# Kernel tuning notes

Hardware: AMD Instinct MI355X
Metric: run time of the kernel (lower is better)

## Reference

```python
import jax, jax.numpy as jnp
import numpy as np


def gcn_conv(x, src, dst, W, b, n_nodes):
    """PyG-style GCNConv: add self-loops, symmetric deg^-1/2 normalization,
    linear transform, scatter-add aggregation to dst, then bias."""
    loop = jnp.arange(n_nodes, dtype=src.dtype)
    s = jnp.concatenate([src, loop])
    d = jnp.concatenate([dst, loop])
    deg = jax.ops.segment_sum(jnp.ones_like(d, x.dtype), d, num_segments=n_nodes)
    dinv = jax.lax.rsqrt(deg)  # deg >= 1 due to self-loops
    norm = dinv[s] * dinv[d]  # [E+N]
    h = x @ W.T  # [N, out]
    msg = h[s] * norm[:, None]  # [E+N, out]
    return jax.ops.segment_sum(msg, d, num_segments=n_nodes) + b


def setup_inputs() -> dict:
    key = jax.random.key(0)
    k = jax.random.split(key, 6)
    N, E, IN, HID, OUT = 100000, 1600000, 128, 128, 64
    x = jax.random.normal(k[0], (N, IN), dtype=jnp.float32)
    edge_index = jax.random.randint(k[1], (2, E), 0, N, dtype=jnp.int64)
    W1 = jax.random.normal(k[2], (HID, IN), dtype=jnp.float32) * 0.05
    b1 = jnp.zeros((HID,), dtype=jnp.float32)
    W2 = jax.random.normal(k[3], (OUT, HID), dtype=jnp.float32) * 0.05
    b2 = jnp.zeros((OUT,), dtype=jnp.float32)
    return {"x": x, "W1": W1, "b1": b1, "W2": W2, "b2": b2, "edge_index": edge_index}


def reference(x, W1, b1, W2, b2, edge_index):
    n_nodes = x.shape[0]
    src, dst = edge_index[0], edge_index[1]
    h = jax.nn.relu(gcn_conv(x, src, dst, W1, b1, n_nodes))
    return gcn_conv(h, src, dst, W2, b2, n_nodes)
```

## Files before the change

### kernel.cpp

```cpp
#include <hip/hip_runtime.h>
#include <hip/hip_bf16.h>


#define IN_F  128
#define HID_F 128
#define OUT_F 64

#define NPB     512
#define MAXBKT  256
#define CHUNK   4096
#define SLAB    12288
#define CAP     12288

typedef __bf16 bf16_t;
typedef __bf16 bf16x4 __attribute__((ext_vector_type(4)));
typedef __bf16 bf16x8 __attribute__((ext_vector_type(8)));
typedef float  f32x2  __attribute__((ext_vector_type(2)));
typedef float  f32x4  __attribute__((ext_vector_type(4)));
typedef unsigned u32x2 __attribute__((ext_vector_type(2)));
typedef unsigned u32x4 __attribute__((ext_vector_type(4)));

__global__ __launch_bounds__(256) void k_hist(const int* __restrict__ dst, int E,
                                              int* __restrict__ chunkhist, int NBKT,
                                              int pchunks,
                                              const float* __restrict__ W1s,
                                              const float* __restrict__ W2s,
                                              bf16_t* __restrict__ Wdst,
                                              int n1, int n2,
                                              int* __restrict__ bcur) {
    if ((int)blockIdx.x >= pchunks) {
        int i = (blockIdx.x - pchunks) * 256 + threadIdx.x;
        if (i < n1) Wdst[i] = (bf16_t)W1s[i];
        else if (i < n1 + n2) Wdst[i] = (bf16_t)W2s[i - n1];
        else if (i < n1 + n2 + NBKT) bcur[(i - n1 - n2) * 16] = (i - n1 - n2) * SLAB;
        return;
    }
    __shared__ int cnt[MAXBKT];
    for (int i = threadIdx.x; i < NBKT; i += 256) cnt[i] = 0;
    __syncthreads();
    int base = blockIdx.x * CHUNK;
    for (int i = threadIdx.x; i < CHUNK; i += 256) {
        int e = base + i;
        if (e < E) atomicAdd(&cnt[dst[e] >> 9], 1);
    }
    __syncthreads();
    int* ch = chunkhist + (size_t)blockIdx.x * MAXBKT;
    for (int i = threadIdx.x; i < NBKT; i += 256) ch[i] = cnt[i];
}

__global__ __launch_bounds__(256) void k_part(const int* __restrict__ src,
                                              const int* __restrict__ dst, int E,
                                              int* __restrict__ bcur,
                                              const int* __restrict__ chunkhist,
                                              unsigned* __restrict__ part, int NBKT) {
    __shared__ int cnt[MAXBKT];
    __shared__ int base[MAXBKT];
    const int* ch = chunkhist + (size_t)blockIdx.x * MAXBKT;
    int off = (int)((blockIdx.x * 73u) % (unsigned)NBKT);
    for (int j = threadIdx.x; j < NBKT; j += 256) {
        int i = j + off; if (i >= NBKT) i -= NBKT;
        int c = ch[i];
        base[i] = c ? atomicAdd(&bcur[i * 16], c) : 0;
        cnt[i] = 0;
    }
    __syncthreads();
    int cbase = blockIdx.x * CHUNK;
    for (int i = threadIdx.x; i < CHUNK; i += 256) {
        int e = cbase + i;
        if (e < E) {
            int d = dst[e];
            int b = d >> 9;
            int lp = atomicAdd(&cnt[b], 1);
            part[base[b] + lp] = (unsigned)src[e] | ((unsigned)(d & 511) << 17);
        }
    }
}

__global__ __launch_bounds__(256) void k_bucket(const unsigned* __restrict__ part,
                                                const int* __restrict__ bcur,
                                                int2* __restrict__ off2,
                                                int* __restrict__ col,
                                                float* __restrict__ dinv, int N) {
    __shared__ int lcnt[NPB];
    __shared__ int lexc[NPB];
    __shared__ int lcur[NPB];
    __shared__ int psum[256];
    __shared__ int stage[CAP];
    int b = blockIdx.x;
    int t = threadIdx.x;
    int node0 = b * NPB;
    int e0s = b * SLAB;
    int cnt = bcur[b * 16] - e0s;
    for (int i = t; i < NPB; i += 256) lcnt[i] = 0;
    __syncthreads();
    for (int i = t; i < cnt; i += 256)
        atomicAdd(&lcnt[part[e0s + i] >> 17], 1);
    __syncthreads();
    int n2b = t * 2;
    int pc0 = (lcnt[n2b] + 7) & ~7;
    int pc1 = (lcnt[n2b + 1] + 7) & ~7;
    psum[t] = pc0 + pc1;
    __syncthreads();
    for (int ofs = 1; ofs < 256; ofs <<= 1) {
        int add = (t >= ofs) ? psum[t - ofs] : 0;
        __syncthreads();
        psum[t] += add;
        __syncthreads();
    }
    int run = (t > 0) ? psum[t - 1] : 0;
    {
        lexc[n2b] = run; lcur[n2b] = run;
        int node = node0 + n2b;
        if (node < N) {
            off2[node] = make_int2(e0s + run, e0s + run + pc0);
            dinv[node] = rsqrtf((float)lcnt[n2b] + 1.0f);
        }
        run += pc0;
        lexc[n2b + 1] = run; lcur[n2b + 1] = run;
        node = node0 + n2b + 1;
        if (node < N) {
            off2[node] = make_int2(e0s + run, e0s + run + pc1);
            dinv[node] = rsqrtf((float)lcnt[n2b + 1] + 1.0f);
        }
    }
    __syncthreads();
    for (int i = t; i < cnt; i += 256) {
        unsigned p = part[e0s + i];
        int dl = p >> 17;
        int sv = (int)(p & 0x1FFFF);
        int lp = atomicAdd(&lcur[dl], 1);
        if (lp < CAP) stage[lp] = sv;
        else col[e0s + lp] = sv;
    }
    __syncthreads();
#pragma unroll
    for (int j = 0; j < 2; j++) {
        int idx = n2b + j;
        int en = lexc[idx] + ((lcnt[idx] + 7) & ~7);
        for (int i = lcur[idx]; i < en; i++) {
            if (i < CAP) stage[i] = N; else col[e0s + i] = N;
        }
    }
    __syncthreads();
    int tot = psum[255];
    for (int i = t; i < tot && i < CAP; i += 256) col[e0s + i] = stage[i];
}

template <int NCOL, typename TIN>
__global__ __launch_bounds__(256) void k_gemm_mfma(const TIN* __restrict__ X,
                                                   const bf16_t* __restrict__ W,
                                                   const float* __restrict__ scale,
                                                   bf16_t* __restrict__ H, int N) {
    constexpr int CT = NCOL / 16;
    int wv = threadIdx.x >> 6, lane = threadIdx.x & 63;
    int quad = lane >> 4, l16 = lane & 15;
    int row0 = blockIdx.x * 128 + wv * 32;
    f32x4 acc[2][CT] = {};
#pragma unroll
    for (int ks = 0; ks < 4; ks++) {
        int k0 = ks * 32 + quad * 8;
        bf16x8 a[2];
#pragma unroll
        for (int rt = 0; rt < 2; rt++) {
            int r = row0 + rt * 16 + l16;
            if (r >= N) r = N - 1;
            const TIN* p = X + (size_t)r * 128 + k0;
            if constexpr (sizeof(TIN) == 4) {
                f32x4 x0 = *(const f32x4*)p;
                f32x4 x1 = *(const f32x4*)(p + 4);
                bf16x8 tt;
                tt[0] = (bf16_t)x0[0]; tt[1] = (bf16_t)x0[1];
                tt[2] = (bf16_t)x0[2]; tt[3] = (bf16_t)x0[3];
                tt[4] = (bf16_t)x1[0]; tt[5] = (bf16_t)x1[1];
                tt[6] = (bf16_t)x1[2]; tt[7] = (bf16_t)x1[3];
                a[rt] = tt;
            } else {
                a[rt] = *(const bf16x8*)p;
            }
        }
#pragma unroll
        for (int ct = 0; ct < CT; ct++) {
            bf16x8 bfrag = *(const bf16x8*)(W + (size_t)(ct * 16 + l16) * 128 + k0);
#pragma unroll
            for (int rt = 0; rt < 2; rt++)
                acc[rt][ct] = __builtin_amdgcn_mfma_f32_16x16x32_bf16(a[rt], bfrag, acc[rt][ct], 0, 0, 0);
        }
    }
#pragma unroll
    for (int rt = 0; rt < 2; rt++)
#pragma unroll
        for (int r4 = 0; r4 < 4; r4++) {
            int r = row0 + rt * 16 + quad * 4 + r4;
            if (r < N) {
                float sc = scale[r];
#pragma unroll
                for (int ct = 0; ct < CT; ct++)
                    H[(size_t)r * NCOL + ct * 16 + l16] = (bf16_t)(sc * acc[rt][ct][r4]);
            } else if (r == N) {
#pragma unroll
                for (int ct = 0; ct < CT; ct++)
                    H[(size_t)N * NCOL + ct * 16 + l16] = (bf16_t)0.f;
            }
        }
}

template <int ROWE>
__device__ __forceinline__ void gather8(const bf16_t* __restrict__ hp,
                                        const int* __restrict__ col, int e,
                                        u32x4* w) {
    int4 c0 = *(const int4*)(col + e);
    int4 c1 = *(const int4*)(col + e + 4);
    w[0] = *(const u32x4*)(hp + (unsigned)c0.x * (unsigned)ROWE);
    w[1] = *(const u32x4*)(hp + (unsigned)c0.y * (unsigned)ROWE);
    w[2] = *(const u32x4*)(hp + (unsigned)c0.z * (unsigned)ROWE);
    w[3] = *(const u32x4*)(hp + (unsigned)c0.w * (unsigned)ROWE);
    w[4] = *(const u32x4*)(hp + (unsigned)c1.x * (unsigned)ROWE);
    w[5] = *(const u32x4*)(hp + (unsigned)c1.y * (unsigned)ROWE);
    w[6] = *(const u32x4*)(hp + (unsigned)c1.z * (unsigned)ROWE);
    w[7] = *(const u32x4*)(hp + (unsigned)c1.w * (unsigned)ROWE);
}

__device__ __forceinline__ void accum8(const u32x4* w, f32x2* a2) {
#pragma unroll
    for (int u = 0; u < 8; u++)
#pragma unroll
        for (int k = 0; k < 4; k++) {
            f32x2 v;
            v.x = __uint_as_float(w[u][k] << 16);
            v.y = __uint_as_float(w[u][k] & 0xffff0000u);
            a2[k] += v;
        }
}

__global__ __launch_bounds__(256) void k_agg_gemm(const bf16_t* __restrict__ h,
                                                  const int2* __restrict__ off2,
                                                  const int* __restrict__ col,
                                                  const float* __restrict__ dinv,
                                                  const float* __restrict__ bias,
                                                  const bf16_t* __restrict__ W2,
                                                  bf16_t* __restrict__ h2, int N) {
    __shared__ float hl[16][132];
    __shared__ float dl[16];
    int lane = threadIdx.x & 63;
    int wv = threadIdx.x >> 6;
    int g = lane >> 4, fl = lane & 15;
    int node0 = blockIdx.x * 16;
    int node = node0 + wv * 4 + g;
    bool alive = node < N;
    int f = fl * 8;
    const bf16_t* hp = h + f;
    f32x2 a2[4] = {};
    float di = 0.f;
    if (alive) {
        u32x4 ws = *(const u32x4*)(hp + (unsigned)node * 128u);
        int2 oe = off2[node];
        di = dinv[node];
#pragma unroll
        for (int k = 0; k < 4; k++) {
            f32x2 v;
            v.x = __uint_as_float(ws[k] << 16);
            v.y = __uint_as_float(ws[k] & 0xffff0000u);
            a2[k] = v;
        }
        u32x4 w[8];
        for (int e = oe.x; e < oe.y; e += 8) {
            gather8<128>(hp, col, e, w);
            accum8(w, a2);
        }
    }
    f32x4 b0 = *(const f32x4*)(bias + f);
    f32x4 b1 = *(const f32x4*)(bias + f + 4);
    int lr = wv * 4 + g;
#pragma unroll
    for (int j = 0; j < 8; j++) {
        float bv = (j < 4) ? b0[j] : b1[j - 4];
        float val = a2[j >> 1][j & 1] * di + bv;
        hl[lr][f + j] = fmaxf(val, 0.f);
    }
    if (fl == 0) dl[lr] = di;
    __syncthreads();

    int quad = lane >> 4, l16 = lane & 15;
    f32x4 c4 = {0.f, 0.f, 0.f, 0.f};
#pragma unroll
    for (int ks = 0; ks < 4; ks++) {
        int k0 = ks * 32 + quad * 8;
        bf16x8 afr;
#pragma unroll
        for (int j = 0; j < 8; j++) afr[j] = (bf16_t)hl[l16][k0 + j];
        bf16x8 bfr = *(const bf16x8*)(W2 + (size_t)(wv * 16 + l16) * 128 + k0);
        c4 = __builtin_amdgcn_mfma_f32_16x16x32_bf16(afr, bfr, c4, 0, 0, 0);
    }
#pragma unroll
    for (int r4 = 0; r4 < 4; r4++) {
        int rr = quad * 4 + r4;
        int gn = node0 + rr;
        if (gn < N)
            h2[(size_t)gn * 64 + wv * 16 + l16] = (bf16_t)(dl[rr] * c4[r4]);
    }
    if (blockIdx.x == 0 && threadIdx.x < 32)
        ((unsigned*)h2)[(size_t)N * 32 + threadIdx.x] = 0u;
}

template <int ROWE, int LPN, bool RELU, typename TOUT>
__global__ __launch_bounds__(256) void k_agg(const bf16_t* __restrict__ h,
                                             const int2* __restrict__ off2,
                                             const int* __restrict__ col,
                                             const float* __restrict__ dinv,
                                             const float* __restrict__ bias,
                                             TOUT* __restrict__ out, int N) {
    constexpr int NPW = 64 / LPN;
    int lane = threadIdx.x & 63;
    int wv = threadIdx.x >> 6;
    int g = lane / LPN, fl = lane % LPN;
    int node = blockIdx.x * (4 * NPW) + wv * NPW + g;
    if (node >= N) return;
    int f = fl * 8;
    const bf16_t* hp = h + f;
    u32x4 ws = *(const u32x4*)(hp + (unsigned)node * (unsigned)ROWE);
    int2 oe = off2[node];
    float di = dinv[node];
    f32x2 a2[4];
#pragma unroll
    for (int k = 0; k < 4; k++) {
        f32x2 v;
        v.x = __uint_as_float(ws[k] << 16);
        v.y = __uint_as_float(ws[k] & 0xffff0000u);
        a2[k] = v;
    }
    u32x4 w[8];
    for (int e = oe.x; e < oe.y; e += 8) {
        gather8<ROWE>(hp, col, e, w);
        accum8(w, a2);
    }
    f32x4 b0 = *(const f32x4*)(bias + f);
    f32x4 b1 = *(const f32x4*)(bias + f + 4);
    float r[8];
#pragma unroll
    for (int j = 0; j < 8; j++) {
        float bv = (j < 4) ? b0[j] : b1[j - 4];
        float val = a2[j >> 1][j & 1] * di + bv;
        if (RELU) val = fmaxf(val, 0.f);
        r[j] = val;
    }
    if constexpr (sizeof(TOUT) == 2) {
        bf16x8 v;
#pragma unroll
        for (int j = 0; j < 8; j++) v[j] = (bf16_t)r[j];
        *(bf16x8*)((bf16_t*)out + (size_t)node * ROWE + f) = v;
    } else {
        f32x4 v0 = {r[0], r[1], r[2], r[3]};
        f32x4 v1 = {r[4], r[5], r[6], r[7]};
        *(f32x4*)((float*)out + (size_t)node * ROWE + f) = v0;
        *(f32x4*)((float*)out + (size_t)node * ROWE + f + 4) = v1;
    }
}

extern "C" void kernel_launch(void* const* d_in, const int* in_sizes, int n_in,
                              void* d_out, int out_size, void* d_ws, size_t ws_size,
                              hipStream_t stream) {
    const float* x  = (const float*)d_in[0];
    const float* W1 = (const float*)d_in[1];
    const float* b1 = (const float*)d_in[2];
    const float* W2 = (const float*)d_in[3];
    const float* b2 = (const float*)d_in[4];
    const int*   ei = (const int*)d_in[5];

    int N = in_sizes[0] / IN_F;
    int E = in_sizes[5] / 2;
    const int* src = ei;
    const int* dst = ei + E;
    int NBKT = (N + NPB - 1) / NPB;
    int pchunks = (E + CHUNK - 1) / CHUNK;

    size_t woff = 0;
    auto alloc = [&](size_t bytes) {
        void* p = (char*)d_ws + woff;
        woff += (bytes + 255) & ~(size_t)255;
        return p;
    };
    int*      bcur  = (int*)alloc((size_t)NBKT * 16 * 4);
    int*      chist = (int*)alloc((size_t)pchunks * MAXBKT * 4);
    unsigned* part  = (unsigned*)alloc((size_t)NBKT * SLAB * 4);
    int*      col   = (int*)alloc((size_t)NBKT * SLAB * 4);
    int2*     off2  = (int2*)alloc((size_t)N * 8);
    float*    dinv  = (float*)alloc((size_t)N * 4);
    bf16_t*   Wb    = (bf16_t*)alloc((size_t)(HID_F * IN_F + OUT_F * HID_F) * 2);
    bf16_t*   W1b   = Wb;
    bf16_t*   W2b   = Wb + HID_F * IN_F;
    bf16_t*   h1    = (bf16_t*)alloc((size_t)(N + 1) * HID_F * 2);
    bf16_t*   h2b   = (bf16_t*)alloc((size_t)(N + 1) * OUT_F * 2);
    float*    outp  = (float*)d_out;

    int n1 = HID_F * IN_F, n2 = OUT_F * HID_F;
    int tailblocks = (n1 + n2 + NBKT + 255) / 256;
    k_hist<<<pchunks + tailblocks, 256, 0, stream>>>(dst, E, chist, NBKT, pchunks,
                                                     W1, W2, Wb, n1, n2, bcur);
    k_part<<<pchunks, 256, 0, stream>>>(src, dst, E, bcur, chist, part, NBKT);
    k_bucket<<<NBKT, 256, 0, stream>>>(part, bcur, off2, col, dinv, N);

    int gemm_blocks = (N + 127) / 128;

    k_gemm_mfma<HID_F, float><<<gemm_blocks, 256, 0, stream>>>(x, W1b, dinv, h1, N);
    k_agg_gemm<<<(N + 15) / 16, 256, 0, stream>>>(h1, off2, col, dinv, b1, W2b, h2b, N);
    k_agg<OUT_F, 8, false, float><<<(N + 31) / 32, 256, 0, stream>>>(h2b, off2, col, dinv, b2, outp, N);
}
```

Measured before the change: 266.2 us.

## Fuse histogram into partition kernel, drop weight pre-cast, widen bucket blocks

Removes the separate histogram kernel by recomputing per-chunk bucket counts inside k_part before reserving slab space with atomics, and replaces the bcur init with a memset. Weights are now read as fp32 and converted to bf16 inside the GEMM kernels instead of in a pre-pass. k_bucket uses 512 threads so each thread owns one node. This saves a launch and the chunk-histogram traffic, at the cost of reading dst twice in k_part and extra conversion work and fp32 weight loads in the GEMMs.

Result: slower. 271.6 us (+2.1%).

```diff
diff --git a/kernel.cpp b/kernel.cpp
--- a/kernel.cpp
+++ b/kernel.cpp
@@ -20,63 +20,36 @@
 typedef unsigned u32x2 __attribute__((ext_vector_type(2)));
 typedef unsigned u32x4 __attribute__((ext_vector_type(4)));
 
-__global__ __launch_bounds__(256) void k_hist(const int* __restrict__ dst, int E,
-                                              int* __restrict__ chunkhist, int NBKT,
-                                              int pchunks,
-                                              const float* __restrict__ W1s,
-                                              const float* __restrict__ W2s,
-                                              bf16_t* __restrict__ Wdst,
-                                              int n1, int n2,
-                                              int* __restrict__ bcur) {
-    if ((int)blockIdx.x >= pchunks) {
-        int i = (blockIdx.x - pchunks) * 256 + threadIdx.x;
-        if (i < n1) Wdst[i] = (bf16_t)W1s[i];
-        else if (i < n1 + n2) Wdst[i] = (bf16_t)W2s[i - n1];
-        else if (i < n1 + n2 + NBKT) bcur[(i - n1 - n2) * 16] = (i - n1 - n2) * SLAB;
-        return;
-    }
-    __shared__ int cnt[MAXBKT];
-    for (int i = threadIdx.x; i < NBKT; i += 256) cnt[i] = 0;
-    __syncthreads();
-    int base = blockIdx.x * CHUNK;
-    for (int i = threadIdx.x; i < CHUNK; i += 256) {
-        int e = base + i;
-        if (e < E) atomicAdd(&cnt[dst[e] >> 9], 1);
-    }
-    __syncthreads();
-    int* ch = chunkhist + (size_t)blockIdx.x * MAXBKT;
-    for (int i = threadIdx.x; i < NBKT; i += 256) ch[i] = cnt[i];
-}
-
 __global__ __launch_bounds__(256) void k_part(const int* __restrict__ src,
                                               const int* __restrict__ dst, int E,
                                               int* __restrict__ bcur,
-                                              const int* __restrict__ chunkhist,
                                               unsigned* __restrict__ part, int NBKT) {
     __shared__ int cnt[MAXBKT];
     __shared__ int base[MAXBKT];
-    const int* ch = chunkhist + (size_t)blockIdx.x * MAXBKT;
+    for (int i = threadIdx.x; i < NBKT; i += 256) cnt[i] = 0;
+    __syncthreads();
+    int cbase = blockIdx.x * CHUNK;
+    int cend = min(cbase + CHUNK, E);
+    for (int e = cbase + (int)threadIdx.x; e < cend; e += 256)
+        atomicAdd(&cnt[dst[e] >> 9], 1);
+    __syncthreads();
     int off = (int)((blockIdx.x * 73u) % (unsigned)NBKT);
     for (int j = threadIdx.x; j < NBKT; j += 256) {
         int i = j + off; if (i >= NBKT) i -= NBKT;
-        int c = ch[i];
-        base[i] = c ? atomicAdd(&bcur[i * 16], c) : 0;
+        int c = cnt[i];
+        base[i] = c ? (i * SLAB + atomicAdd(&bcur[i * 16], c)) : 0;
         cnt[i] = 0;
     }
     __syncthreads();
-    int cbase = blockIdx.x * CHUNK;
-    for (int i = threadIdx.x; i < CHUNK; i += 256) {
-        int e = cbase + i;
-        if (e < E) {
-            int d = dst[e];
-            int b = d >> 9;
-            int lp = atomicAdd(&cnt[b], 1);
-            part[base[b] + lp] = (unsigned)src[e] | ((unsigned)(d & 511) << 17);
-        }
-    }
-}
-
-__global__ __launch_bounds__(256) void k_bucket(const unsigned* __restrict__ part,
+    for (int e = cbase + (int)threadIdx.x; e < cend; e += 256) {
+        int d = dst[e];
+        int b = d >> 9;
+        int lp = atomicAdd(&cnt[b], 1);
+        part[base[b] + lp] = (unsigned)src[e] | ((unsigned)(d & 511) << 17);
+    }
+}
+
+__global__ __launch_bounds__(512) void k_bucket(const unsigned* __restrict__ part,
                                                 const int* __restrict__ bcur,
                                                 int2* __restrict__ off2,
                                                 int* __restrict__ col,
@@ -84,47 +57,37 @@
     __shared__ int lcnt[NPB];
     __shared__ int lexc[NPB];
     __shared__ int lcur[NPB];
-    __shared__ int psum[256];
+    __shared__ int psum[NPB];
     __shared__ int stage[CAP];
     int b = blockIdx.x;
     int t = threadIdx.x;
     int node0 = b * NPB;
     int e0s = b * SLAB;
-    int cnt = bcur[b * 16] - e0s;
-    for (int i = t; i < NPB; i += 256) lcnt[i] = 0;
-    __syncthreads();
-    for (int i = t; i < cnt; i += 256)
+    int cnt = bcur[b * 16];
+    lcnt[t] = 0;
+    __syncthreads();
+    for (int i = t; i < cnt; i += 512)
         atomicAdd(&lcnt[part[e0s + i] >> 17], 1);
     __syncthreads();
-    int n2b = t * 2;
-    int pc0 = (lcnt[n2b] + 7) & ~7;
-    int pc1 = (lcnt[n2b + 1] + 7) & ~7;
-    psum[t] = pc0 + pc1;
-    __syncthreads();
-    for (int ofs = 1; ofs < 256; ofs <<= 1) {
+    int pc = (lcnt[t] + 7) & ~7;
+    psum[t] = pc;
+    __syncthreads();
+    for (int ofs = 1; ofs < NPB; ofs <<= 1) {
         int add = (t >= ofs) ? psum[t - ofs] : 0;
         __syncthreads();
         psum[t] += add;
         __syncthreads();
     }
-    int run = (t > 0) ? psum[t - 1] : 0;
-    {
-        lexc[n2b] = run; lcur[n2b] = run;
-        int node = node0 + n2b;
-        if (node < N) {
-            off2[node] = make_int2(e0s + run, e0s + run + pc0);
-            dinv[node] = rsqrtf((float)lcnt[n2b] + 1.0f);
-        }
-        run += pc0;
-        lexc[n2b + 1] = run; lcur[n2b + 1] = run;
-        node = node0 + n2b + 1;
-        if (node < N) {
-            off2[node] = make_int2(e0s + run, e0s + run + pc1);
-            dinv[node] = rsqrtf((float)lcnt[n2b + 1] + 1.0f);
-        }
-    }
-    __syncthreads();
-    for (int i = t; i < cnt; i += 256) {
+    int run = psum[t] - pc;
+    lexc[t] = run;
+    lcur[t] = run;
+    int node = node0 + t;
+    if (node < N) {
+        off2[node] = make_int2(e0s + run, e0s + run + pc);
+        dinv[node] = rsqrtf((float)lcnt[t] + 1.0f);
+    }
+    __syncthreads();
+    for (int i = t; i < cnt; i += 512) {
         unsigned p = part[e0s + i];
         int dl = p >> 17;
         int sv = (int)(p & 0x1FFFF);
@@ -133,22 +96,20 @@
         else col[e0s + lp] = sv;
     }
     __syncthreads();
-#pragma unroll
-    for (int j = 0; j < 2; j++) {
-        int idx = n2b + j;
-        int en = lexc[idx] + ((lcnt[idx] + 7) & ~7);
-        for (int i = lcur[idx]; i < en; i++) {
+    {
+        int en = lexc[t] + pc;
+        for (int i = lcur[t]; i < en; i++) {
             if (i < CAP) stage[i] = N; else col[e0s + i] = N;
         }
     }
     __syncthreads();
-    int tot = psum[255];
-    for (int i = t; i < tot && i < CAP; i += 256) col[e0s + i] = stage[i];
+    int tot = psum[NPB - 1];
+    for (int i = t; i < tot && i < CAP; i += 512) col[e0s + i] = stage[i];
 }
 
 template <int NCOL, typename TIN>
 __global__ __launch_bounds__(256) void k_gemm_mfma(const TIN* __restrict__ X,
-                                                   const bf16_t* __restrict__ W,
+                                                   const float* __restrict__ W,
                                                    const float* __restrict__ scale,
                                                    bf16_t* __restrict__ H, int N) {
     constexpr int CT = NCOL / 16;
@@ -180,7 +141,14 @@
         }
 #pragma unroll
         for (int ct = 0; ct < CT; ct++) {
-            bf16x8 bfrag = *(const bf16x8*)(W + (size_t)(ct * 16 + l16) * 128 + k0);
+            const float* wp = W + (size_t)(ct * 16 + l16) * 128 + k0;
+            f32x4 w0 = *(const f32x4*)wp;
+            f32x4 w1 = *(const f32x4*)(wp + 4);
+            bf16x8 bfrag;
+            bfrag[0] = (bf16_t)w0[0]; bfrag[1] = (bf16_t)w0[1];
+            bfrag[2] = (bf16_t)w0[2]; bfrag[3] = (bf16_t)w0[3];
+            bfrag[4] = (bf16_t)w1[0]; bfrag[5] = (bf16_t)w1[1];
+            bfrag[6] = (bf16_t)w1[2]; bfrag[7] = (bf16_t)w1[3];
 #pragma unroll
             for (int rt = 0; rt < 2; rt++)
                 acc[rt][ct] = __builtin_amdgcn_mfma_f32_16x16x32_bf16(a[rt], bfrag, acc[rt][ct], 0, 0, 0);
@@ -237,7 +205,7 @@
                                                   const int* __restrict__ col,
                                                   const float* __restrict__ dinv,
                                                   const float* __restrict__ bias,
-                                                  const bf16_t* __restrict__ W2,
+                                                  const float* __restrict__ W2,
                                                   bf16_t* __restrict__ h2, int N) {
     __shared__ float hl[16][132];
     __shared__ float dl[16];
@@ -288,7 +256,14 @@
         bf16x8 afr;
 #pragma unroll
         for (int j = 0; j < 8; j++) afr[j] = (bf16_t)hl[l16][k0 + j];
-        bf16x8 bfr = *(const bf16x8*)(W2 + (size_t)(wv * 16 + l16) * 128 + k0);
+        const float* wp = W2 + (size_t)(wv * 16 + l16) * 128 + k0;
+        f32x4 w0 = *(const f32x4*)wp;
+        f32x4 w1 = *(const f32x4*)(wp + 4);
+        bf16x8 bfr;
+        bfr[0] = (bf16_t)w0[0]; bfr[1] = (bf16_t)w0[1];
+        bfr[2] = (bf16_t)w0[2]; bfr[3] = (bf16_t)w0[3];
+        bfr[4] = (bf16_t)w1[0]; bfr[5] = (bf16_t)w1[1];
+        bfr[6] = (bf16_t)w1[2]; bfr[7] = (bf16_t)w1[3];
         c4 = __builtin_amdgcn_mfma_f32_16x16x32_bf16(afr, bfr, c4, 0, 0, 0);
     }
 #pragma unroll
@@ -380,28 +355,21 @@
         return p;
     };
     int*      bcur  = (int*)alloc((size_t)NBKT * 16 * 4);
-    int*      chist = (int*)alloc((size_t)pchunks * MAXBKT * 4);
     unsigned* part  = (unsigned*)alloc((size_t)NBKT * SLAB * 4);
     int*      col   = (int*)alloc((size_t)NBKT * SLAB * 4);
     int2*     off2  = (int2*)alloc((size_t)N * 8);
     float*    dinv  = (float*)alloc((size_t)N * 4);
-    bf16_t*   Wb    = (bf16_t*)alloc((size_t)(HID_F * IN_F + OUT_F * HID_F) * 2);
-    bf16_t*   W1b   = Wb;
-    bf16_t*   W2b   = Wb + HID_F * IN_F;
     bf16_t*   h1    = (bf16_t*)alloc((size_t)(N + 1) * HID_F * 2);
     bf16_t*   h2b   = (bf16_t*)alloc((size_t)(N + 1) * OUT_F * 2);
     float*    outp  = (float*)d_out;
 
-    int n1 = HID_F * IN_F, n2 = OUT_F * HID_F;
-    int tailblocks = (n1 + n2 + NBKT + 255) / 256;
-    k_hist<<<pchunks + tailblocks, 256, 0, stream>>>(dst, E, chist, NBKT, pchunks,
-                                                     W1, W2, Wb, n1, n2, bcur);
-    k_part<<<pchunks, 256, 0, stream>>>(src, dst, E, bcur, chist, part, NBKT);
-    k_bucket<<<NBKT, 256, 0, stream>>>(part, bcur, off2, col, dinv, N);
+    hipMemsetAsync(bcur, 0, (size_t)NBKT * 16 * 4, stream);
+    k_part<<<pchunks, 256, 0, stream>>>(src, dst, E, bcur, part, NBKT);
+    k_bucket<<<NBKT, 512, 0, stream>>>(part, bcur, off2, col, dinv, N);
 
     int gemm_blocks = (N + 127) / 128;
 
-    k_gemm_mfma<HID_F, float><<<gemm_blocks, 256, 0, stream>>>(x, W1b, dinv, h1, N);
-    k_agg_gemm<<<(N + 15) / 16, 256, 0, stream>>>(h1, off2, col, dinv, b1, W2b, h2b, N);
+    k_gemm_mfma<HID_F, float><<<gemm_blocks, 256, 0, stream>>>(x, W1, dinv, h1, N);
+    k_agg_gemm<<<(N + 15) / 16, 256, 0, stream>>>(h1, off2, col, dinv, b1, W2, h2b, N);
     k_agg<OUT_F, 8, false, float><<<(N + 31) / 32, 256, 0, stream>>>(h2b, off2, col, dinv, b2, outp, N);
 }
```
